# Kernel tuning notes

Measured on AMD Instinct MI355X. Metric: run time of the kernel, lower is better.

Reference implementation:

```python
import jax, jax.numpy as jnp
import numpy as np

B, C, N, K = 8, 64, 16384, 8
MLPS = [128, 128, 256]
IN_CH = C * K + K  # 520


def setup_inputs() -> dict:
    key = jax.random.key(0)
    ks = jax.random.split(key, 10)
    feature = jax.random.normal(ks[0], (B, C, N), jnp.float32)
    idx = jax.random.randint(ks[1], (B, N, K), 0, N)
    dis = jax.random.uniform(ks[2], (B, N, K), jnp.float32)
    # MlpConv parameters: conv1x1 layers IN_CH -> 128 -> 128 -> 256
    dims = [IN_CH] + MLPS
    params = {}
    for i in range(len(MLPS)):
        params[f"W{i+1}"] = jax.random.normal(ks[3 + i], (dims[i + 1], dims[i]), jnp.float32) * 0.02
        params[f"b{i+1}"] = jnp.zeros((dims[i + 1],), jnp.float32)
    return dict(feature=feature, idx=idx, dis=dis, **params)


def _forward(feature, idx, dis, W1, b1, W2, b2, W3, b3):
    # group: gather neighbor features -> [B, C, N, K]
    grouped = jax.vmap(lambda f, i: f[:, i])(feature, idx)
    g = jnp.transpose(grouped, (0, 2, 3, 1))            # [B, N, K, C]
    g = jnp.concatenate([dis[..., None], g], axis=3)    # [B, N, K, C+1]
    g = g.reshape(B, N, K * (C + 1))                    # [B, N, K*(C+1)]
    x = jnp.transpose(g, (0, 2, 1))                     # [B, IN_CH, N]
    # MlpConv: conv1x1 stack, ReLU between layers, no activation on last
    for W, b, last in ((W1, b1, False), (W2, b2, False), (W3, b3, True)):
        x = jnp.einsum('bcn,oc->bon', x, W) + b[:, None]
        if not last:
            x = jax.nn.relu(x)
    return x


def reference(feature, idx, dis, W1, b1, W2, b2, W3, b3):
    return _forward(feature, idx, dis, W1, b1, W2, b2, W3, b3)
```

## Files before the change

kernel.cpp:

```cpp
#include <hip/hip_runtime.h>
#include <hip/hip_bf16.h>
#include <stdint.h>

#define BB 8
#define CC 64
#define NN 16384
#define KNB 8

typedef __attribute__((ext_vector_type(8))) short   s16x8;
typedef __attribute__((ext_vector_type(4))) short   s16x4;
typedef __attribute__((ext_vector_type(8))) __bf16  bf16x8;
typedef __attribute__((ext_vector_type(4))) float   f32x4;

__device__ __forceinline__ unsigned short f2bf(float f) {
    unsigned u = __builtin_bit_cast(unsigned, f);
    u = (u + 0x7FFFu + ((u >> 16) & 1u)) >> 16;
    return (unsigned short)u;
}

__device__ __forceinline__ int getq(const int4& q, int j) {
    return j == 0 ? q.x : j == 1 ? q.y : j == 2 ? q.z : q.w;
}

#define OFF_DISB  16777216u
#define OFF_W1B   18874368u
#define OFF_W2B   19013632u
#define OFF_W3B   19046400u

__global__ __launch_bounds__(256) void prep_all(
    const float* __restrict__ feat, const float* __restrict__ dis,
    const float* __restrict__ W1, const float* __restrict__ W2, const float* __restrict__ W3,
    unsigned short* __restrict__ featT, unsigned short* __restrict__ disB,
    unsigned short* __restrict__ w1p, unsigned short* __restrict__ w2p,
    unsigned short* __restrict__ w3p)
{
    const int bid = blockIdx.x;
    if (bid < 512) {
        int gt = bid * 256 + threadIdx.x;
        int b = gt >> 14, n = gt & 16383;
        const float* fp = feat + ((size_t)b << 20) + n;
        unsigned short v[64];
        #pragma unroll
        for (int c = 0; c < 64; ++c) v[c] = f2bf(fp[(size_t)c << 14]);
        unsigned short* dst = featT + (size_t)gt * 64;
        #pragma unroll
        for (int j = 0; j < 8; ++j) {
            s16x8 pk;
            #pragma unroll
            for (int i = 0; i < 8; ++i) pk[i] = (short)v[j * 8 + i];
            *(s16x8*)(dst + j * 8) = pk;
        }
        return;
    }
    int tid = (bid - 512) * 256 + threadIdx.x;
    if (tid < 131072) {
        const float* dp = dis + (size_t)tid * 8;
        s16x8 pk;
        #pragma unroll
        for (int j = 0; j < 8; ++j) pk[j] = (short)f2bf(dp[j]);
        *(s16x8*)(disB + (size_t)tid * 8) = pk;
        return;
    }
    int t2 = tid - 131072;
    if (t2 < 8704) {
        int kb   = t2 >> 9;
        int rem  = t2 & 511;
        int t    = rem >> 6;
        int lane = rem & 63;
        int row  = t * 16 + (lane & 15);
        int kbase = kb * 32 + (lane >> 4) * 8;
        s16x8 pk;
        #pragma unroll
        for (int j = 0; j < 8; ++j) {
            int kp = kbase + j;
            float val = 0.f;
            if (kp < 512) {
                int kk = kp >> 6, c = kp & 63;
                val = W1[row * 520 + kk * 65 + 1 + c];
            } else if (kp < 520) {
                val = W1[row * 520 + (kp - 512) * 65];
            }
            pk[j] = (short)f2bf(val);
        }
        *(s16x8*)(w1p + (size_t)t2 * 8) = pk;
    } else if (t2 < 8704 + 2048) {
        int f    = t2 - 8704;
        int kb   = f >> 9;
        int rem  = f & 511;
        int t    = rem >> 6;
        int lane = rem & 63;
        int row  = t * 16 + (lane & 15);
        int k    = kb * 32 + (lane >> 4) * 8;
        s16x8 pk;
        #pragma unroll
        for (int j = 0; j < 8; ++j) pk[j] = (short)f2bf(W2[row * 128 + k + j]);
        *(s16x8*)(w2p + (size_t)f * 8) = pk;
    } else if (t2 < 8704 + 2048 + 4096) {
        int f    = t2 - 10752;
        int hk   = f >> 9;
        int half = hk >> 2, kb = hk & 3;
        int rem  = f & 511;
        int t    = rem >> 6;
        int lane = rem & 63;
        int row  = (half * 8 + t) * 16 + (lane & 15);
        int k    = kb * 32 + (lane >> 4) * 8;
        s16x8 pk;
        #pragma unroll
        for (int j = 0; j < 8; ++j) pk[j] = (short)f2bf(W3[row * 128 + k + j]);
        *(s16x8*)(w3p + (size_t)f * 8) = pk;
    }
}

__device__ __forceinline__ void wload4(const unsigned short* wp, int frag0, int lane,
                                       bf16x8& w0, bf16x8& w1, bf16x8& w2, bf16x8& w3)
{
    w0 = *(const bf16x8*)(wp + (size_t)((frag0 + 0) * 64 + lane) * 8);
    w1 = *(const bf16x8*)(wp + (size_t)((frag0 + 1) * 64 + lane) * 8);
    w2 = *(const bf16x8*)(wp + (size_t)((frag0 + 2) * 64 + lane) * 8);
    w3 = *(const bf16x8*)(wp + (size_t)((frag0 + 3) * 64 + lane) * 8);
}

template <int KB>
__device__ __forceinline__ void gather4(const unsigned short* featB, const int4 (&iq)[4],
                                        int grp8, bf16x8& G0, bf16x8& G1, bf16x8& G2, bf16x8& G3)
{
    constexpr int kk = KB >> 1;
    constexpr int j  = kk & 3;
    const int c0 = (KB & 1) * 32 + grp8;
    G0 = *(const bf16x8*)(featB + (((size_t)(unsigned)getq(iq[0], j)) << 6) + c0);
    G1 = *(const bf16x8*)(featB + (((size_t)(unsigned)getq(iq[1], j)) << 6) + c0);
    G2 = *(const bf16x8*)(featB + (((size_t)(unsigned)getq(iq[2], j)) << 6) + c0);
    G3 = *(const bf16x8*)(featB + (((size_t)(unsigned)getq(iq[3], j)) << 6) + c0);
}

__device__ __forceinline__ void refresh_iq(int4 (&iq)[4], const int* ip0) {
    #pragma unroll
    for (int pt = 0; pt < 4; ++pt) iq[pt] = *(const int4*)(ip0 + pt * 128 + 4);
}

__device__ __forceinline__ void disload4(const unsigned short* disB, int p0, int l15, int grp,
                                         bf16x8& G0, bf16x8& G1, bf16x8& G2, bf16x8& G3)
{
    const s16x8 z = {0,0,0,0,0,0,0,0};
    if (grp == 0) {
        G0 = *(const bf16x8*)(disB + (size_t)(p0 +  0 + l15) * 8);
        G1 = *(const bf16x8*)(disB + (size_t)(p0 + 16 + l15) * 8);
        G2 = *(const bf16x8*)(disB + (size_t)(p0 + 32 + l15) * 8);
        G3 = *(const bf16x8*)(disB + (size_t)(p0 + 48 + l15) * 8);
    } else {
        G0 = __builtin_bit_cast(bf16x8, z); G1 = __builtin_bit_cast(bf16x8, z);
        G2 = __builtin_bit_cast(bf16x8, z); G3 = __builtin_bit_cast(bf16x8, z);
    }
}

__device__ __forceinline__ void dsread4(const unsigned short* strip, int kb, int l15, int grp8,
                                        bf16x8& G0, bf16x8& G1, bf16x8& G2, bf16x8& G3)
{
    G0 = *(const bf16x8*)(strip + (0 * 16 + l15) * 136 + kb * 32 + grp8);
    G1 = *(const bf16x8*)(strip + (1 * 16 + l15) * 136 + kb * 32 + grp8);
    G2 = *(const bf16x8*)(strip + (2 * 16 + l15) * 136 + kb * 32 + grp8);
    G3 = *(const bf16x8*)(strip + (3 * 16 + l15) * 136 + kb * 32 + grp8);
}

__device__ __forceinline__ void mfma_quad(f32x4 (&ac)[8][4], int t0,
    const bf16x8& wa, const bf16x8& wb, const bf16x8& wc, const bf16x8& wd,
    const bf16x8& B0, const bf16x8& B1, const bf16x8& B2, const bf16x8& B3)
{
    __builtin_amdgcn_s_setprio(1);
    ac[t0+0][0] = __builtin_amdgcn_mfma_f32_16x16x32_bf16(wa, B0, ac[t0+0][0], 0, 0, 0);
    ac[t0+0][1] = __builtin_amdgcn_mfma_f32_16x16x32_bf16(wa, B1, ac[t0+0][1], 0, 0, 0);
    ac[t0+0][2] = __builtin_amdgcn_mfma_f32_16x16x32_bf16(wa, B2, ac[t0+0][2], 0, 0, 0);
    ac[t0+0][3] = __builtin_amdgcn_mfma_f32_16x16x32_bf16(wa, B3, ac[t0+0][3], 0, 0, 0);
    ac[t0+1][0] = __builtin_amdgcn_mfma_f32_16x16x32_bf16(wb, B0, ac[t0+1][0], 0, 0, 0);
    ac[t0+1][1] = __builtin_amdgcn_mfma_f32_16x16x32_bf16(wb, B1, ac[t0+1][1], 0, 0, 0);
    ac[t0+1][2] = __builtin_amdgcn_mfma_f32_16x16x32_bf16(wb, B2, ac[t0+1][2], 0, 0, 0);
    ac[t0+1][3] = __builtin_amdgcn_mfma_f32_16x16x32_bf16(wb, B3, ac[t0+1][3], 0, 0, 0);
    ac[t0+2][0] = __builtin_amdgcn_mfma_f32_16x16x32_bf16(wc, B0, ac[t0+2][0], 0, 0, 0);
    ac[t0+2][1] = __builtin_amdgcn_mfma_f32_16x16x32_bf16(wc, B1, ac[t0+2][1], 0, 0, 0);
    ac[t0+2][2] = __builtin_amdgcn_mfma_f32_16x16x32_bf16(wc, B2, ac[t0+2][2], 0, 0, 0);
    ac[t0+2][3] = __builtin_amdgcn_mfma_f32_16x16x32_bf16(wc, B3, ac[t0+2][3], 0, 0, 0);
    ac[t0+3][0] = __builtin_amdgcn_mfma_f32_16x16x32_bf16(wd, B0, ac[t0+3][0], 0, 0, 0);
    ac[t0+3][1] = __builtin_amdgcn_mfma_f32_16x16x32_bf16(wd, B1, ac[t0+3][1], 0, 0, 0);
    ac[t0+3][2] = __builtin_amdgcn_mfma_f32_16x16x32_bf16(wd, B2, ac[t0+3][2], 0, 0, 0);
    ac[t0+3][3] = __builtin_amdgcn_mfma_f32_16x16x32_bf16(wd, B3, ac[t0+3][3], 0, 0, 0);
    __builtin_amdgcn_s_setprio(0);
}

__global__ __launch_bounds__(64, 2) void pointconv_main(
    const unsigned short* __restrict__ featT,
    const unsigned short* __restrict__ disB,
    const int* __restrict__ idx,
    const unsigned short* __restrict__ w1p,
    const unsigned short* __restrict__ w2p,
    const unsigned short* __restrict__ w3p,
    const float* __restrict__ b1, const float* __restrict__ b2,
    const float* __restrict__ b3, float* __restrict__ out)
{
    __shared__ __align__(16) unsigned short strip[64 * 136];
    const int bid  = blockIdx.x;
    const int wg   = (bid & 7) * 256 + (bid >> 3);
    const int lane = threadIdx.x;
    const int grp  = lane >> 4;
    const int grp8 = grp * 8;
    const int l15  = lane & 15;
    const int p0   = wg * 64;
    const int b    = p0 >> 14;
    const int n0   = p0 & 16383;

    bf16x8 gA0, gA1, gA2, gA3, gB0, gB1, gB2, gB3;
    bf16x8 wA0, wA1, wA2, wA3, wB0, wB1, wB2, wB3;

    wload4(w1p, 0, lane, wA0, wA1, wA2, wA3);

    const int* ip0 = idx + (size_t)(p0 + l15) * 8;
    int4 iq[4];
    #pragma unroll
    for (int pt = 0; pt < 4; ++pt) iq[pt] = *(const int4*)(ip0 + pt * 128);

    const unsigned short* featB = featT + ((size_t)b << 20);

    gather4<0>(featB, iq, grp8, gA0, gA1, gA2, gA3);
    gather4<1>(featB, iq, grp8, gB0, gB1, gB2, gB3);

    f32x4 acc[8][4];
    #pragma unroll
    for (int t = 0; t < 8; ++t)
        #pragma unroll
        for (int pt = 0; pt < 4; ++pt) acc[t][pt] = (f32x4){0.f, 0.f, 0.f, 0.f};

#define G1_BODY(KB, S0,S1,S2,S3, WNEXT, GNEXT)                              \
    wload4(w1p, (KB)*8 + 4, lane, wB0, wB1, wB2, wB3);                      \
    mfma_quad(acc, 0, wA0, wA1, wA2, wA3, S0, S1, S2, S3);                  \
    WNEXT;                                                                  \
    mfma_quad(acc, 4, wB0, wB1, wB2, wB3, S0, S1, S2, S3);                  \
    GNEXT;

    G1_BODY(0,  gA0,gA1,gA2,gA3, wload4(w1p,  8, lane, wA0,wA1,wA2,wA3), (gather4< 2>(featB, iq, grp8, gA0,gA1,gA2,gA3)))
    G1_BODY(1,  gB0,gB1,gB2,gB3, wload4(w1p, 16, lane, wA0,wA1,wA2,wA3), (gather4< 3>(featB, iq, grp8, gB0,gB1,gB2,gB3)))
    G1_BODY(2,  gA0,gA1,gA2,gA3, wload4(w1p, 24, lane, wA0,wA1,wA2,wA3), (gather4< 4>(featB, iq, grp8, gA0,gA1,gA2,gA3)))
    G1_BODY(3,  gB0,gB1,gB2,gB3, wload4(w1p, 32, lane, wA0,wA1,wA2,wA3), (gather4< 5>(featB, iq, grp8, gB0,gB1,gB2,gB3)))
    G1_BODY(4,  gA0,gA1,gA2,gA3, wload4(w1p, 40, lane, wA0,wA1,wA2,wA3), (gather4< 6>(featB, iq, grp8, gA0,gA1,gA2,gA3)))
    G1_BODY(5,  gB0,gB1,gB2,gB3, wload4(w1p, 48, lane, wA0,wA1,wA2,wA3), (gather4< 7>(featB, iq, grp8, gB0,gB1,gB2,gB3)))
    refresh_iq(iq, ip0);
    G1_BODY(6,  gA0,gA1,gA2,gA3, wload4(w1p, 56, lane, wA0,wA1,wA2,wA3), (gather4< 8>(featB, iq, grp8, gA0,gA1,gA2,gA3)))
    G1_BODY(7,  gB0,gB1,gB2,gB3, wload4(w1p, 64, lane, wA0,wA1,wA2,wA3), (gather4< 9>(featB, iq, grp8, gB0,gB1,gB2,gB3)))
    G1_BODY(8,  gA0,gA1,gA2,gA3, wload4(w1p, 72, lane, wA0,wA1,wA2,wA3), (gather4<10>(featB, iq, grp8, gA0,gA1,gA2,gA3)))
    G1_BODY(9,  gB0,gB1,gB2,gB3, wload4(w1p, 80, lane, wA0,wA1,wA2,wA3), (gather4<11>(featB, iq, grp8, gB0,gB1,gB2,gB3)))
    G1_BODY(10, gA0,gA1,gA2,gA3, wload4(w1p, 88, lane, wA0,wA1,wA2,wA3), (gather4<12>(featB, iq, grp8, gA0,gA1,gA2,gA3)))
    G1_BODY(11, gB0,gB1,gB2,gB3, wload4(w1p, 96, lane, wA0,wA1,wA2,wA3), (gather4<13>(featB, iq, grp8, gB0,gB1,gB2,gB3)))
    G1_BODY(12, gA0,gA1,gA2,gA3, wload4(w1p,104, lane, wA0,wA1,wA2,wA3), (gather4<14>(featB, iq, grp8, gA0,gA1,gA2,gA3)))
    G1_BODY(13, gB0,gB1,gB2,gB3, wload4(w1p,112, lane, wA0,wA1,wA2,wA3), (gather4<15>(featB, iq, grp8, gB0,gB1,gB2,gB3)))
    G1_BODY(14, gA0,gA1,gA2,gA3, wload4(w1p,120, lane, wA0,wA1,wA2,wA3), disload4(disB, p0, l15, grp, gA0,gA1,gA2,gA3))
    G1_BODY(15, gB0,gB1,gB2,gB3, wload4(w1p,128, lane, wA0,wA1,wA2,wA3), )
    G1_BODY(16, gA0,gA1,gA2,gA3, wload4(w2p, 0, lane, wA0,wA1,wA2,wA3), )
#undef G1_BODY

    #pragma unroll
    for (int t = 0; t < 8; ++t) {
        const int chb = t * 16 + grp * 4;
        const float4 bv = *(const float4*)(b1 + chb);
        #pragma unroll
        for (int pt = 0; pt < 4; ++pt) {
            s16x4 pk;
            float v0 = acc[t][pt][0] + bv.x; pk[0] = (short)f2bf(v0 > 0.f ? v0 : 0.f);
            float v1 = acc[t][pt][1] + bv.y; pk[1] = (short)f2bf(v1 > 0.f ? v1 : 0.f);
            float v2 = acc[t][pt][2] + bv.z; pk[2] = (short)f2bf(v2 > 0.f ? v2 : 0.f);
            float v3 = acc[t][pt][3] + bv.w; pk[3] = (short)f2bf(v3 > 0.f ? v3 : 0.f);
            *(s16x4*)(strip + (pt * 16 + l15) * 136 + chb) = pk;
        }
    }

    f32x4 acc2[8][4];
    #pragma unroll
    for (int t = 0; t < 8; ++t)
        #pragma unroll
        for (int pt = 0; pt < 4; ++pt) acc2[t][pt] = (f32x4){0.f, 0.f, 0.f, 0.f};

    dsread4(strip, 0, l15, grp8, gA0, gA1, gA2, gA3);

#define G23_BODY(WP, FR, S0,S1,S2,S3, ACC, WNEXT, DSNEXT)                   \
    wload4(WP, (FR) + 4, lane, wB0, wB1, wB2, wB3);                         \
    mfma_quad(ACC, 0, wA0, wA1, wA2, wA3, S0, S1, S2, S3);                  \
    WNEXT;                                                                  \
    DSNEXT;                                                                 \
    mfma_quad(ACC, 4, wB0, wB1, wB2, wB3, S0, S1, S2, S3);

    G23_BODY(w2p,  0, gA0,gA1,gA2,gA3, acc2, wload4(w2p,  8, lane, wA0,wA1,wA2,wA3), dsread4(strip, 1, l15, grp8, gB0,gB1,gB2,gB3))
    G23_BODY(w2p,  8, gB0,gB1,gB2,gB3, acc2, wload4(w2p, 16, lane, wA0,wA1,wA2,wA3), dsread4(strip, 2, l15, grp8, gA0,gA1,gA2,gA3))
    G23_BODY(w2p, 16, gA0,gA1,gA2,gA3, acc2, wload4(w2p, 24, lane, wA0,wA1,wA2,wA3), dsread4(strip, 3, l15, grp8, gB0,gB1,gB2,gB3))
    G23_BODY(w2p, 24, gB0,gB1,gB2,gB3, acc2, wload4(w3p,  0, lane, wA0,wA1,wA2,wA3), )

    #pragma unroll
    for (int t = 0; t < 8; ++t) {
        const int chb = t * 16 + grp * 4;
        const float4 bv = *(const float4*)(b2 + chb);
        #pragma unroll
        for (int pt = 0; pt < 4; ++pt) {
            s16x4 pk;
            float v0 = acc2[t][pt][0] + bv.x; pk[0] = (short)f2bf(v0 > 0.f ? v0 : 0.f);
            float v1 = acc2[t][pt][1] + bv.y; pk[1] = (short)f2bf(v1 > 0.f ? v1 : 0.f);
            float v2 = acc2[t][pt][2] + bv.z; pk[2] = (short)f2bf(v2 > 0.f ? v2 : 0.f);
            float v3 = acc2[t][pt][3] + bv.w; pk[3] = (short)f2bf(v3 > 0.f ? v3 : 0.f);
            *(s16x4*)(strip + (pt * 16 + l15) * 136 + chb) = pk;
        }
    }

    #pragma unroll
    for (int half = 0; half < 2; ++half) {
        f32x4 acc3[8][4];
        #pragma unroll
        for (int t = 0; t < 8; ++t)
            #pragma unroll
            for (int pt = 0; pt < 4; ++pt) acc3[t][pt] = (f32x4){0.f, 0.f, 0.f, 0.f};

        dsread4(strip, 0, l15, grp8, gA0, gA1, gA2, gA3);
        if (half == 0) {
            G23_BODY(w3p,  0, gA0,gA1,gA2,gA3, acc3, wload4(w3p,  8, lane, wA0,wA1,wA2,wA3), dsread4(strip, 1, l15, grp8, gB0,gB1,gB2,gB3))
            G23_BODY(w3p,  8, gB0,gB1,gB2,gB3, acc3, wload4(w3p, 16, lane, wA0,wA1,wA2,wA3), dsread4(strip, 2, l15, grp8, gA0,gA1,gA2,gA3))
            G23_BODY(w3p, 16, gA0,gA1,gA2,gA3, acc3, wload4(w3p, 24, lane, wA0,wA1,wA2,wA3), dsread4(strip, 3, l15, grp8, gB0,gB1,gB2,gB3))
            G23_BODY(w3p, 24, gB0,gB1,gB2,gB3, acc3, wload4(w3p, 32, lane, wA0,wA1,wA2,wA3), )
        } else {
            G23_BODY(w3p, 32, gA0,gA1,gA2,gA3, acc3, wload4(w3p, 40, lane, wA0,wA1,wA2,wA3), dsread4(strip, 1, l15, grp8, gB0,gB1,gB2,gB3))
            G23_BODY(w3p, 40, gB0,gB1,gB2,gB3, acc3, wload4(w3p, 48, lane, wA0,wA1,wA2,wA3), dsread4(strip, 2, l15, grp8, gA0,gA1,gA2,gA3))
            G23_BODY(w3p, 48, gA0,gA1,gA2,gA3, acc3, wload4(w3p, 56, lane, wA0,wA1,wA2,wA3), dsread4(strip, 3, l15, grp8, gB0,gB1,gB2,gB3))
            G23_BODY(w3p, 56, gB0,gB1,gB2,gB3, acc3, , )
        }

        #pragma unroll
        for (int t = 0; t < 8; ++t) {
            const int chb = half * 128 + t * 16 + grp * 4;
            const float4 bv = *(const float4*)(b3 + chb);
            #pragma unroll
            for (int pt = 0; pt < 4; ++pt) {
                const int n = n0 + pt * 16 + l15;
                float* op = out + (((size_t)(b * 256 + chb)) << 14) + n;
                op[0]                  = acc3[t][pt][0] + bv.x;
                op[(size_t)1 << 14]    = acc3[t][pt][1] + bv.y;
                op[(size_t)2 << 14]    = acc3[t][pt][2] + bv.z;
                op[(size_t)3 << 14]    = acc3[t][pt][3] + bv.w;
            }
        }
    }
#undef G23_BODY
}

extern "C" void kernel_launch(void* const* d_in, const int* in_sizes, int n_in,
                              void* d_out, int out_size, void* d_ws, size_t ws_size,
                              hipStream_t stream)
{
    const float* feature = (const float*)d_in[0];
    const int*   idx     = (const int*)d_in[1];
    const float* dis     = (const float*)d_in[2];
    const float* W1      = (const float*)d_in[3];
    const float* b1      = (const float*)d_in[4];
    const float* W2      = (const float*)d_in[5];
    const float* b2      = (const float*)d_in[6];
    const float* W3      = (const float*)d_in[7];
    const float* b3      = (const float*)d_in[8];
    float* out = (float*)d_out;

    char* ws = (char*)d_ws;
    unsigned short* featT = (unsigned short*)ws;
    unsigned short* disB  = (unsigned short*)(ws + OFF_DISB);
    unsigned short* w1p   = (unsigned short*)(ws + OFF_W1B);
    unsigned short* w2p   = (unsigned short*)(ws + OFF_W2B);
    unsigned short* w3p   = (unsigned short*)(ws + OFF_W3B);

    hipLaunchKernelGGL(prep_all, dim3(1488), dim3(256), 0, stream,
                       feature, dis, W1, W2, W3, featT, disB, w1p, w2p, w3p);
    hipLaunchKernelGGL(pointconv_main, dim3(2048), dim3(64), 0, stream,
                       featT, disB, idx, w1p, w2p, w3p, b1, b2, b3, out);
}
```

Baseline: 73.07 us.

## Split output channels across two waves per block with shared LDS strip

Each 64-point block now runs two wavefronts instead of one, each computing half of the output channels for every layer. Per-wave accumulator tiles shrink from 8x4 to 4x4, which lowers register pressure, and the launch bound allows three blocks per CU. Both waves duplicate the neighbor gather loads, and barriers are added around the shared LDS strip between layers. The intent is more latency hiding and occupancy, paid for with redundant gathers and synchronization.

```diff
diff --git a/kernel.cpp b/kernel.cpp
--- a/kernel.cpp
+++ b/kernel.cpp
@@ -162,31 +162,31 @@
     G3 = *(const bf16x8*)(strip + (3 * 16 + l15) * 136 + kb * 32 + grp8);
 }
 
-__device__ __forceinline__ void mfma_quad(f32x4 (&ac)[8][4], int t0,
-    const bf16x8& wa, const bf16x8& wb, const bf16x8& wc, const bf16x8& wd,
+__device__ __forceinline__ void mfma_q4(f32x4 (&ac)[4][4],
+    const bf16x8& w0, const bf16x8& w1, const bf16x8& w2, const bf16x8& w3,
     const bf16x8& B0, const bf16x8& B1, const bf16x8& B2, const bf16x8& B3)
 {
     __builtin_amdgcn_s_setprio(1);
-    ac[t0+0][0] = __builtin_amdgcn_mfma_f32_16x16x32_bf16(wa, B0, ac[t0+0][0], 0, 0, 0);
-    ac[t0+0][1] = __builtin_amdgcn_mfma_f32_16x16x32_bf16(wa, B1, ac[t0+0][1], 0, 0, 0);
-    ac[t0+0][2] = __builtin_amdgcn_mfma_f32_16x16x32_bf16(wa, B2, ac[t0+0][2], 0, 0, 0);
-    ac[t0+0][3] = __builtin_amdgcn_mfma_f32_16x16x32_bf16(wa, B3, ac[t0+0][3], 0, 0, 0);
-    ac[t0+1][0] = __builtin_amdgcn_mfma_f32_16x16x32_bf16(wb, B0, ac[t0+1][0], 0, 0, 0);
-    ac[t0+1][1] = __builtin_amdgcn_mfma_f32_16x16x32_bf16(wb, B1, ac[t0+1][1], 0, 0, 0);
-    ac[t0+1][2] = __builtin_amdgcn_mfma_f32_16x16x32_bf16(wb, B2, ac[t0+1][2], 0, 0, 0);
-    ac[t0+1][3] = __builtin_amdgcn_mfma_f32_16x16x32_bf16(wb, B3, ac[t0+1][3], 0, 0, 0);
-    ac[t0+2][0] = __builtin_amdgcn_mfma_f32_16x16x32_bf16(wc, B0, ac[t0+2][0], 0, 0, 0);
-    ac[t0+2][1] = __builtin_amdgcn_mfma_f32_16x16x32_bf16(wc, B1, ac[t0+2][1], 0, 0, 0);
-    ac[t0+2][2] = __builtin_amdgcn_mfma_f32_16x16x32_bf16(wc, B2, ac[t0+2][2], 0, 0, 0);
-    ac[t0+2][3] = __builtin_amdgcn_mfma_f32_16x16x32_bf16(wc, B3, ac[t0+2][3], 0, 0, 0);
-    ac[t0+3][0] = __builtin_amdgcn_mfma_f32_16x16x32_bf16(wd, B0, ac[t0+3][0], 0, 0, 0);
-    ac[t0+3][1] = __builtin_amdgcn_mfma_f32_16x16x32_bf16(wd, B1, ac[t0+3][1], 0, 0, 0);
-    ac[t0+3][2] = __builtin_amdgcn_mfma_f32_16x16x32_bf16(wd, B2, ac[t0+3][2], 0, 0, 0);
-    ac[t0+3][3] = __builtin_amdgcn_mfma_f32_16x16x32_bf16(wd, B3, ac[t0+3][3], 0, 0, 0);
+    ac[0][0] = __builtin_amdgcn_mfma_f32_16x16x32_bf16(w0, B0, ac[0][0], 0, 0, 0);
+    ac[0][1] = __builtin_amdgcn_mfma_f32_16x16x32_bf16(w0, B1, ac[0][1], 0, 0, 0);
+    ac[0][2] = __builtin_amdgcn_mfma_f32_16x16x32_bf16(w0, B2, ac[0][2], 0, 0, 0);
+    ac[0][3] = __builtin_amdgcn_mfma_f32_16x16x32_bf16(w0, B3, ac[0][3], 0, 0, 0);
+    ac[1][0] = __builtin_amdgcn_mfma_f32_16x16x32_bf16(w1, B0, ac[1][0], 0, 0, 0);
+    ac[1][1] = __builtin_amdgcn_mfma_f32_16x16x32_bf16(w1, B1, ac[1][1], 0, 0, 0);
+    ac[1][2] = __builtin_amdgcn_mfma_f32_16x16x32_bf16(w1, B2, ac[1][2], 0, 0, 0);
+    ac[1][3] = __builtin_amdgcn_mfma_f32_16x16x32_bf16(w1, B3, ac[1][3], 0, 0, 0);
+    ac[2][0] = __builtin_amdgcn_mfma_f32_16x16x32_bf16(w2, B0, ac[2][0], 0, 0, 0);
+    ac[2][1] = __builtin_amdgcn_mfma_f32_16x16x32_bf16(w2, B1, ac[2][1], 0, 0, 0);
+    ac[2][2] = __builtin_amdgcn_mfma_f32_16x16x32_bf16(w2, B2, ac[2][2], 0, 0, 0);
+    ac[2][3] = __builtin_amdgcn_mfma_f32_16x16x32_bf16(w2, B3, ac[2][3], 0, 0, 0);
+    ac[3][0] = __builtin_amdgcn_mfma_f32_16x16x32_bf16(w3, B0, ac[3][0], 0, 0, 0);
+    ac[3][1] = __builtin_amdgcn_mfma_f32_16x16x32_bf16(w3, B1, ac[3][1], 0, 0, 0);
+    ac[3][2] = __builtin_amdgcn_mfma_f32_16x16x32_bf16(w3, B2, ac[3][2], 0, 0, 0);
+    ac[3][3] = __builtin_amdgcn_mfma_f32_16x16x32_bf16(w3, B3, ac[3][3], 0, 0, 0);
     __builtin_amdgcn_s_setprio(0);
 }
 
-__global__ __launch_bounds__(64, 2) void pointconv_main(
+__global__ __launch_bounds__(128, 3) void pointconv_main(
     const unsigned short* __restrict__ featT,
     const unsigned short* __restrict__ disB,
     const int* __restrict__ idx,
@@ -199,7 +199,10 @@
     __shared__ __align__(16) unsigned short strip[64 * 136];
     const int bid  = blockIdx.x;
     const int wg   = (bid & 7) * 256 + (bid >> 3);
-    const int lane = threadIdx.x;
+    const int tid  = threadIdx.x;
+    const int wv   = tid >> 6;
+    const int tw   = wv * 4;
+    const int lane = tid & 63;
     const int grp  = lane >> 4;
     const int grp8 = grp * 8;
     const int l15  = lane & 15;
@@ -210,7 +213,7 @@
     bf16x8 gA0, gA1, gA2, gA3, gB0, gB1, gB2, gB3;
     bf16x8 wA0, wA1, wA2, wA3, wB0, wB1, wB2, wB3;
 
-    wload4(w1p, 0, lane, wA0, wA1, wA2, wA3);
+    wload4(w1p, 0 * 8 + tw, lane, wA0, wA1, wA2, wA3);
 
     const int* ip0 = idx + (size_t)(p0 + l15) * 8;
     int4 iq[4];
@@ -222,42 +225,46 @@
     gather4<0>(featB, iq, grp8, gA0, gA1, gA2, gA3);
     gather4<1>(featB, iq, grp8, gB0, gB1, gB2, gB3);
 
-    f32x4 acc[8][4];
-    #pragma unroll
-    for (int t = 0; t < 8; ++t)
+    f32x4 acc[4][4];
+    #pragma unroll
+    for (int t = 0; t < 4; ++t)
         #pragma unroll
         for (int pt = 0; pt < 4; ++pt) acc[t][pt] = (f32x4){0.f, 0.f, 0.f, 0.f};
 
-#define G1_BODY(KB, S0,S1,S2,S3, WNEXT, GNEXT)                              \
-    wload4(w1p, (KB)*8 + 4, lane, wB0, wB1, wB2, wB3);                      \
-    mfma_quad(acc, 0, wA0, wA1, wA2, wA3, S0, S1, S2, S3);                  \
-    WNEXT;                                                                  \
-    mfma_quad(acc, 4, wB0, wB1, wB2, wB3, S0, S1, S2, S3);                  \
+#define G1_E(KB, GNEXT)                                                     \
+    wload4(w1p, (KB + 1) * 8 + tw, lane, wB0, wB1, wB2, wB3);               \
+    mfma_q4(acc, wA0, wA1, wA2, wA3, gA0, gA1, gA2, gA3);                   \
     GNEXT;
-
-    G1_BODY(0,  gA0,gA1,gA2,gA3, wload4(w1p,  8, lane, wA0,wA1,wA2,wA3), (gather4< 2>(featB, iq, grp8, gA0,gA1,gA2,gA3)))
-    G1_BODY(1,  gB0,gB1,gB2,gB3, wload4(w1p, 16, lane, wA0,wA1,wA2,wA3), (gather4< 3>(featB, iq, grp8, gB0,gB1,gB2,gB3)))
-    G1_BODY(2,  gA0,gA1,gA2,gA3, wload4(w1p, 24, lane, wA0,wA1,wA2,wA3), (gather4< 4>(featB, iq, grp8, gA0,gA1,gA2,gA3)))
-    G1_BODY(3,  gB0,gB1,gB2,gB3, wload4(w1p, 32, lane, wA0,wA1,wA2,wA3), (gather4< 5>(featB, iq, grp8, gB0,gB1,gB2,gB3)))
-    G1_BODY(4,  gA0,gA1,gA2,gA3, wload4(w1p, 40, lane, wA0,wA1,wA2,wA3), (gather4< 6>(featB, iq, grp8, gA0,gA1,gA2,gA3)))
-    G1_BODY(5,  gB0,gB1,gB2,gB3, wload4(w1p, 48, lane, wA0,wA1,wA2,wA3), (gather4< 7>(featB, iq, grp8, gB0,gB1,gB2,gB3)))
+#define G1_O(KB, GNEXT)                                                     \
+    wload4(w1p, (KB + 1) * 8 + tw, lane, wA0, wA1, wA2, wA3);               \
+    mfma_q4(acc, wB0, wB1, wB2, wB3, gB0, gB1, gB2, gB3);                   \
+    GNEXT;
+
+    G1_E(0,  (gather4< 2>(featB, iq, grp8, gA0,gA1,gA2,gA3)))
+    G1_O(1,  (gather4< 3>(featB, iq, grp8, gB0,gB1,gB2,gB3)))
+    G1_E(2,  (gather4< 4>(featB, iq, grp8, gA0,gA1,gA2,gA3)))
+    G1_O(3,  (gather4< 5>(featB, iq, grp8, gB0,gB1,gB2,gB3)))
+    G1_E(4,  (gather4< 6>(featB, iq, grp8, gA0,gA1,gA2,gA3)))
+    G1_O(5,  (gather4< 7>(featB, iq, grp8, gB0,gB1,gB2,gB3)))
     refresh_iq(iq, ip0);
-    G1_BODY(6,  gA0,gA1,gA2,gA3, wload4(w1p, 56, lane, wA0,wA1,wA2,wA3), (gather4< 8>(featB, iq, grp8, gA0,gA1,gA2,gA3)))
-    G1_BODY(7,  gB0,gB1,gB2,gB3, wload4(w1p, 64, lane, wA0,wA1,wA2,wA3), (gather4< 9>(featB, iq, grp8, gB0,gB1,gB2,gB3)))
-    G1_BODY(8,  gA0,gA1,gA2,gA3, wload4(w1p, 72, lane, wA0,wA1,wA2,wA3), (gather4<10>(featB, iq, grp8, gA0,gA1,gA2,gA3)))
-    G1_BODY(9,  gB0,gB1,gB2,gB3, wload4(w1p, 80, lane, wA0,wA1,wA2,wA3), (gather4<11>(featB, iq, grp8, gB0,gB1,gB2,gB3)))
-    G1_BODY(10, gA0,gA1,gA2,gA3, wload4(w1p, 88, lane, wA0,wA1,wA2,wA3), (gather4<12>(featB, iq, grp8, gA0,gA1,gA2,gA3)))
-    G1_BODY(11, gB0,gB1,gB2,gB3, wload4(w1p, 96, lane, wA0,wA1,wA2,wA3), (gather4<13>(featB, iq, grp8, gB0,gB1,gB2,gB3)))
-    G1_BODY(12, gA0,gA1,gA2,gA3, wload4(w1p,104, lane, wA0,wA1,wA2,wA3), (gather4<14>(featB, iq, grp8, gA0,gA1,gA2,gA3)))
-    G1_BODY(13, gB0,gB1,gB2,gB3, wload4(w1p,112, lane, wA0,wA1,wA2,wA3), (gather4<15>(featB, iq, grp8, gB0,gB1,gB2,gB3)))
-    G1_BODY(14, gA0,gA1,gA2,gA3, wload4(w1p,120, lane, wA0,wA1,wA2,wA3), disload4(disB, p0, l15, grp, gA0,gA1,gA2,gA3))
-    G1_BODY(15, gB0,gB1,gB2,gB3, wload4(w1p,128, lane, wA0,wA1,wA2,wA3), )
-    G1_BODY(16, gA0,gA1,gA2,gA3, wload4(w2p, 0, lane, wA0,wA1,wA2,wA3), )
-#undef G1_BODY
-
-    #pragma unroll
-    for (int t = 0; t < 8; ++t) {
-        const int chb = t * 16 + grp * 4;
+    G1_E(6,  (gather4< 8>(featB, iq, grp8, gA0,gA1,gA2,gA3)))
+    G1_O(7,  (gather4< 9>(featB, iq, grp8, gB0,gB1,gB2,gB3)))
+    G1_E(8,  (gather4<10>(featB, iq, grp8, gA0,gA1,gA2,gA3)))
+    G1_O(9,  (gather4<11>(featB, iq, grp8, gB0,gB1,gB2,gB3)))
+    G1_E(10, (gather4<12>(featB, iq, grp8, gA0,gA1,gA2,gA3)))
+    G1_O(11, (gather4<13>(featB, iq, grp8, gB0,gB1,gB2,gB3)))
+    G1_E(12, (gather4<14>(featB, iq, grp8, gA0,gA1,gA2,gA3)))
+    G1_O(13, (gather4<15>(featB, iq, grp8, gB0,gB1,gB2,gB3)))
+    G1_E(14, disload4(disB, p0, l15, grp, gA0,gA1,gA2,gA3))
+    G1_O(15, )
+    wload4(w2p, 0 * 8 + tw, lane, wB0, wB1, wB2, wB3);
+    mfma_q4(acc, wA0, wA1, wA2, wA3, gA0, gA1, gA2, gA3);
+#undef G1_E
+#undef G1_O
+
+    #pragma unroll
+    for (int t = 0; t < 4; ++t) {
+        const int chb = (tw + t) * 16 + grp * 4;
         const float4 bv = *(const float4*)(b1 + chb);
         #pragma unroll
         for (int pt = 0; pt < 4; ++pt) {
@@ -269,30 +276,33 @@
             *(s16x4*)(strip + (pt * 16 + l15) * 136 + chb) = pk;
         }
     }
-
-    f32x4 acc2[8][4];
-    #pragma unroll
-    for (int t = 0; t < 8; ++t)
+    __syncthreads();
+
+    f32x4 acc2[4][4];
+    #pragma unroll
+    for (int t = 0; t < 4; ++t)
         #pragma unroll
         for (int pt = 0; pt < 4; ++pt) acc2[t][pt] = (f32x4){0.f, 0.f, 0.f, 0.f};
 
     dsread4(strip, 0, l15, grp8, gA0, gA1, gA2, gA3);
 
-#define G23_BODY(WP, FR, S0,S1,S2,S3, ACC, WNEXT, DSNEXT)                   \
-    wload4(WP, (FR) + 4, lane, wB0, wB1, wB2, wB3);                         \
-    mfma_quad(ACC, 0, wA0, wA1, wA2, wA3, S0, S1, S2, S3);                  \
-    WNEXT;                                                                  \
-    DSNEXT;                                                                 \
-    mfma_quad(ACC, 4, wB0, wB1, wB2, wB3, S0, S1, S2, S3);
-
-    G23_BODY(w2p,  0, gA0,gA1,gA2,gA3, acc2, wload4(w2p,  8, lane, wA0,wA1,wA2,wA3), dsread4(strip, 1, l15, grp8, gB0,gB1,gB2,gB3))
-    G23_BODY(w2p,  8, gB0,gB1,gB2,gB3, acc2, wload4(w2p, 16, lane, wA0,wA1,wA2,wA3), dsread4(strip, 2, l15, grp8, gA0,gA1,gA2,gA3))
-    G23_BODY(w2p, 16, gA0,gA1,gA2,gA3, acc2, wload4(w2p, 24, lane, wA0,wA1,wA2,wA3), dsread4(strip, 3, l15, grp8, gB0,gB1,gB2,gB3))
-    G23_BODY(w2p, 24, gB0,gB1,gB2,gB3, acc2, wload4(w3p,  0, lane, wA0,wA1,wA2,wA3), )
-
-    #pragma unroll
-    for (int t = 0; t < 8; ++t) {
-        const int chb = t * 16 + grp * 4;
+    wload4(w2p, 1 * 8 + tw, lane, wA0, wA1, wA2, wA3);
+    dsread4(strip, 1, l15, grp8, gB0, gB1, gB2, gB3);
+    mfma_q4(acc2, wB0, wB1, wB2, wB3, gA0, gA1, gA2, gA3);
+    wload4(w2p, 2 * 8 + tw, lane, wB0, wB1, wB2, wB3);
+    dsread4(strip, 2, l15, grp8, gA0, gA1, gA2, gA3);
+    mfma_q4(acc2, wA0, wA1, wA2, wA3, gB0, gB1, gB2, gB3);
+    wload4(w2p, 3 * 8 + tw, lane, wA0, wA1, wA2, wA3);
+    dsread4(strip, 3, l15, grp8, gB0, gB1, gB2, gB3);
+    mfma_q4(acc2, wB0, wB1, wB2, wB3, gA0, gA1, gA2, gA3);
+    wload4(w3p, tw * 8, lane, wB0, wB1, wB2, wB3);
+    mfma_q4(acc2, wA0, wA1, wA2, wA3, gB0, gB1, gB2, gB3);
+
+    __syncthreads();
+
+    #pragma unroll
+    for (int t = 0; t < 4; ++t) {
+        const int chb = (tw + t) * 16 + grp * 4;
         const float4 bv = *(const float4*)(b2 + chb);
         #pragma unroll
         for (int pt = 0; pt < 4; ++pt) {
@@ -304,36 +314,37 @@
             *(s16x4*)(strip + (pt * 16 + l15) * 136 + chb) = pk;
         }
     }
-
-    #pragma unroll
-    for (int half = 0; half < 2; ++half) {
-        f32x4 acc3[8][4];
-        #pragma unroll
-        for (int t = 0; t < 8; ++t)
+    __syncthreads();
+
+    #pragma unroll
+    for (int p = 0; p < 2; ++p) {
+        f32x4 acc3[4][4];
+        #pragma unroll
+        for (int t = 0; t < 4; ++t)
             #pragma unroll
             for (int pt = 0; pt < 4; ++pt) acc3[t][pt] = (f32x4){0.f, 0.f, 0.f, 0.f};
 
         dsread4(strip, 0, l15, grp8, gA0, gA1, gA2, gA3);
-        if (half == 0) {
-            G23_BODY(w3p,  0, gA0,gA1,gA2,gA3, acc3, wload4(w3p,  8, lane, wA0,wA1,wA2,wA3), dsread4(strip, 1, l15, grp8, gB0,gB1,gB2,gB3))
-            G23_BODY(w3p,  8, gB0,gB1,gB2,gB3, acc3, wload4(w3p, 16, lane, wA0,wA1,wA2,wA3), dsread4(strip, 2, l15, grp8, gA0,gA1,gA2,gA3))
-            G23_BODY(w3p, 16, gA0,gA1,gA2,gA3, acc3, wload4(w3p, 24, lane, wA0,wA1,wA2,wA3), dsread4(strip, 3, l15, grp8, gB0,gB1,gB2,gB3))
-            G23_BODY(w3p, 24, gB0,gB1,gB2,gB3, acc3, wload4(w3p, 32, lane, wA0,wA1,wA2,wA3), )
-        } else {
-            G23_BODY(w3p, 32, gA0,gA1,gA2,gA3, acc3, wload4(w3p, 40, lane, wA0,wA1,wA2,wA3), dsread4(strip, 1, l15, grp8, gB0,gB1,gB2,gB3))
-            G23_BODY(w3p, 40, gB0,gB1,gB2,gB3, acc3, wload4(w3p, 48, lane, wA0,wA1,wA2,wA3), dsread4(strip, 2, l15, grp8, gA0,gA1,gA2,gA3))
-            G23_BODY(w3p, 48, gA0,gA1,gA2,gA3, acc3, wload4(w3p, 56, lane, wA0,wA1,wA2,wA3), dsread4(strip, 3, l15, grp8, gB0,gB1,gB2,gB3))
-            G23_BODY(w3p, 56, gB0,gB1,gB2,gB3, acc3, , )
-        }
-
-        #pragma unroll
-        for (int t = 0; t < 8; ++t) {
-            const int chb = half * 128 + t * 16 + grp * 4;
-            const float4 bv = *(const float4*)(b3 + chb);
+        wload4(w3p, (tw + 1) * 8 + p * 4, lane, wA0, wA1, wA2, wA3);
+        dsread4(strip, 1, l15, grp8, gB0, gB1, gB2, gB3);
+        mfma_q4(acc3, wB0, wB1, wB2, wB3, gA0, gA1, gA2, gA3);
+        wload4(w3p, (tw + 2) * 8 + p * 4, lane, wB0, wB1, wB2, wB3);
+        dsread4(strip, 2, l15, grp8, gA0, gA1, gA2, gA3);
+        mfma_q4(acc3, wA0, wA1, wA2, wA3, gB0, gB1, gB2, gB3);
+        wload4(w3p, (tw + 3) * 8 + p * 4, lane, wA0, wA1, wA2, wA3);
+        dsread4(strip, 3, l15, grp8, gB0, gB1, gB2, gB3);
+        mfma_q4(acc3, wB0, wB1, wB2, wB3, gA0, gA1, gA2, gA3);
+        if (p == 0) wload4(w3p, tw * 8 + 4, lane, wB0, wB1, wB2, wB3);
+        mfma_q4(acc3, wA0, wA1, wA2, wA3, gB0, gB1, gB2, gB3);
+
+        #pragma unroll
+        for (int t = 0; t < 4; ++t) {
+            const int ch0 = wv * 128 + p * 64 + t * 16 + grp * 4;
+            const float4 bv = *(const float4*)(b3 + ch0);
             #pragma unroll
             for (int pt = 0; pt < 4; ++pt) {
                 const int n = n0 + pt * 16 + l15;
-                float* op = out + (((size_t)(b * 256 + chb)) << 14) + n;
+                float* op = out + (((size_t)(b * 256 + ch0)) << 14) + n;
                 op[0]                  = acc3[t][pt][0] + bv.x;
                 op[(size_t)1 << 14]    = acc3[t][pt][1] + bv.y;
                 op[(size_t)2 << 14]    = acc3[t][pt][2] + bv.z;
@@ -341,7 +352,6 @@
             }
         }
     }
-#undef G23_BODY
 }
 
 extern "C" void kernel_launch(void* const* d_in, const int* in_sizes, int n_in,
@@ -368,6 +378,6 @@
 
     hipLaunchKernelGGL(prep_all, dim3(1488), dim3(256), 0, stream,
                        feature, dis, W1, W2, W3, featT, disB, w1p, w2p, w3p);
-    hipLaunchKernelGGL(pointconv_main, dim3(2048), dim3(64), 0, stream,
+    hipLaunchKernelGGL(pointconv_main, dim3(2048), dim3(128), 0, stream,
                        featT, disB, idx, w1p, w2p, w3p, b1, b2, b3, out);
 }
```

Result: slower. 102.5 us (+40.2%).
